# Performance work log

Measured on AMD Instinct MI355X. Metric: run time of the kernel, lower is better.

The kernel has to match this reference:

```python
import jax, jax.numpy as jnp
import numpy as np

N, T, V, F, K, FO = 8, 64, 200, 64, 3, 64


def setup_inputs() -> dict:
    key = jax.random.key(0)
    k1, k2, k3, k4 = jax.random.split(key, 4)
    x = jax.random.normal(k1, (N, T, V, F), dtype=jnp.float32)
    Att = jax.random.uniform(k2, (N, V, V), dtype=jnp.float32)
    S = jax.random.uniform(k3, (N, T, V, V), dtype=jnp.float32)
    Theta = jax.random.normal(k4, (K, F, FO), dtype=jnp.float32) * 0.1
    return {"x": x, "Att": Att, "S": S, "Theta": Theta}


def reference(x, Att, S, Theta):
    # x: (N,T,V,F); Att: (N,V,V); S: (N,T,V,V); Theta: (K,F,FO)
    n, t, v, f = x.shape
    k_order = Theta.shape[0]
    # symmetrize S by elementwise min with its transpose (last two dims)
    S = jnp.minimum(S, jnp.swapaxes(S, -1, -2))
    eye = jnp.eye(v, dtype=x.dtype)
    # D = diag_embed(sum(A, dim=1)) per timestep -> column sums over axis 2
    d = jnp.sum(S, axis=2)                      # (N,T,V)
    L = d[..., :, None] * eye - S               # (N,T,V,V), D - A
    L_t = L - eye                               # tilde-L
    # Chebyshev recursion (elementwise, matching original code exactly)
    polys = [jnp.broadcast_to(eye, (1, 1, v, v)), L_t][:k_order]
    for _ in range(2, k_order):
        polys.append(2.0 * L_t * polys[-1] - polys[-2])
    Att_b = Att[:, None]                        # (N,1,V,V), broadcast over T
    out = jnp.zeros((n, t, v, Theta.shape[-1]), dtype=x.dtype)
    for kk in range(k_order):
        T_k_att = polys[kk] * Att_b             # (N,T,V,V) (broadcast for k=0)
        # rhs = T_k_att^T @ x : sum over vertex u
        rhs = jnp.einsum('...uv,...uf->...vf', T_k_att, x)  # (N,T,V,F)
        out = out + rhs @ Theta[kk]             # (N,T,V,FO)
    return jax.nn.relu(out)
```

## Files before the change

kernel.cpp:

```cpp
#include <hip/hip_runtime.h>

namespace {

typedef __attribute__((ext_vector_type(8)))  short          short8;
typedef __attribute__((ext_vector_type(8)))  unsigned short u16x8;
typedef __attribute__((ext_vector_type(4)))  unsigned short u16x4;
typedef __attribute__((ext_vector_type(4)))  float          f32x4;

constexpr int V  = 200;
constexpr int F  = 64;
constexpr int NT = 512;
constexpr int VP = 208;

constexpr size_t WS_AC  = 0;
constexpr size_t WS_XTF = 95420416;
constexpr size_t WS_THT = 110100480;
constexpr size_t WS_D   = 110125056;
constexpr size_t WS_ADG = 110551040;

__device__ __forceinline__ unsigned short f2bf(float x) {
    union { float f; unsigned u; } c; c.f = x;
    unsigned r = c.u + 0x7FFF + ((c.u >> 16) & 1);
    return (unsigned short)(r >> 16);
}

__global__ __launch_bounds__(256)
void prep_misc(const float* __restrict__ x,
               const float* __restrict__ Theta,
               unsigned short* __restrict__ xTf,
               unsigned short* __restrict__ thT)
{
    __shared__ __align__(16) char smem[30464];
    const int bb = blockIdx.x, tid = threadIdx.x;
    if (bb < NT) {
        unsigned short* xs = (unsigned short*)smem;
        const float* __restrict__ xp = x + (size_t)bb * (V * F);
        for (int idx = tid; idx < 224 * 16; idx += 256) {
            const int u = idx >> 4, fg = idx & 15;
            u16x4 w; w[0] = 0; w[1] = 0; w[2] = 0; w[3] = 0;
            if (u < V) {
                const float4 v4 = *(const float4*)&xp[u * F + 4 * fg];
                w[0] = f2bf(v4.x); w[1] = f2bf(v4.y); w[2] = f2bf(v4.z); w[3] = f2bf(v4.w);
            }
            *(u16x4*)&xs[u * 68 + 4 * fg] = w;
        }
        __syncthreads();
        unsigned short* xo = xTf + (size_t)bb * 14336;
        for (int it = 0; it < 7; ++it) {
            const int wid = tid + 256 * it;
            const int frag = wid >> 6, lane = wid & 63;
            const int kt = frag >> 2, ft = frag & 3;
            const int q = lane >> 4, ln = lane & 15;
            u16x8 w;
            #pragma unroll
            for (int j = 0; j < 8; ++j)
                w[j] = xs[(32 * kt + 8 * q + j) * 68 + 16 * ft + ln];
            *(u16x8*)&xo[frag * 512 + lane * 8] = w;
        }
    } else {
        float* T = (float*)smem;
        for (int k = 0; k < 3; ++k) {
            __syncthreads();
            for (int idx = tid; idx < 4096; idx += 256)
                T[(idx >> 6) * 65 + (idx & 63)] = Theta[k * 4096 + idx];
            __syncthreads();
            for (int idx = tid; idx < 4096; idx += 256) {
                const int fo = idx >> 6, f = idx & 63;
                thT[k * 4096 + fo * 64 + f] = f2bf(T[f * 65 + fo]);
            }
        }
    }
}

__global__ __launch_bounds__(256)
void prep_A(const float* __restrict__ S,
            const float* __restrict__ Att,
            unsigned short* __restrict__ Ac,
            float* __restrict__ d_ws,
            float* __restrict__ adiag)
{
    __shared__ float As[32][33];
    __shared__ float Bs[32][33];
    __shared__ float Ts[32][33];
    __shared__ float Us[32][33];
    __shared__ float Ms[32][33];

    const int b = blockIdx.x, n = b >> 6, tid = threadIdx.x;
    int rem = blockIdx.y, ti = 0;
    while (rem >= 7 - ti) { rem -= 7 - ti; ++ti; }
    const int tj = ti + rem;
    const bool diag = (ti == tj);

    const float* __restrict__ Sp = S   + (size_t)b * (V * V);
    const float* __restrict__ Ap = Att + (size_t)n * (V * V);

    const int r = tid >> 3, cg = tid & 7, c0 = 4 * cg;

    {
        const int gr = 32 * ti + r, gc = 32 * tj + c0;
        float4 a = make_float4(0.f, 0.f, 0.f, 0.f);
        float4 t = make_float4(0.f, 0.f, 0.f, 0.f);
        if (gr < V && gc < V) {
            a = *(const float4*)&Sp[gr * V + gc];
            t = *(const float4*)&Ap[gr * V + gc];
        }
        As[r][c0+0] = a.x; As[r][c0+1] = a.y; As[r][c0+2] = a.z; As[r][c0+3] = a.w;
        Ts[r][c0+0] = t.x; Ts[r][c0+1] = t.y; Ts[r][c0+2] = t.z; Ts[r][c0+3] = t.w;
        if (!diag) {
            const int hr = 32 * tj + r, hc = 32 * ti + c0;
            float4 bb = make_float4(0.f, 0.f, 0.f, 0.f);
            float4 uu = make_float4(0.f, 0.f, 0.f, 0.f);
            if (hr < V && hc < V) {
                bb = *(const float4*)&Sp[hr * V + hc];
                uu = *(const float4*)&Ap[hr * V + hc];
            }
            Bs[r][c0+0] = bb.x; Bs[r][c0+1] = bb.y; Bs[r][c0+2] = bb.z; Bs[r][c0+3] = bb.w;
            Us[r][c0+0] = uu.x; Us[r][c0+1] = uu.y; Us[r][c0+2] = uu.z; Us[r][c0+3] = uu.w;
        }
    }
    __syncthreads();

    {
        float rs = 0.f;
        #pragma unroll
        for (int e = 0; e < 4; ++e) {
            const int c = c0 + e;
            const float tw = diag ? As[c][r] : Bs[c][r];
            const float m = fminf(As[r][c], tw);
            Ms[r][c] = m;
            rs += m;
        }
        rs += __shfl_xor(rs, 1); rs += __shfl_xor(rs, 2); rs += __shfl_xor(rs, 4);
        const int vg = 32 * ti + r;
        if (cg == 0 && vg < V) {
            const float extra = diag ? (-1.0f - As[r][r]) : 0.0f;
            atomicAdd(&d_ws[b * VP + vg], rs + extra);
            if (diag) adiag[n * VP + vg] = Ts[r][r];
        }
    }
    __syncthreads();

    if (!diag) {
        float ts = 0.f;
        #pragma unroll
        for (int e = 0; e < 4; ++e) ts += Ms[c0 + e][r];
        ts += __shfl_xor(ts, 1); ts += __shfl_xor(ts, 2); ts += __shfl_xor(ts, 4);
        if (cg == 0 && 32 * tj + r < V)
            atomicAdd(&d_ws[b * VP + 32 * tj + r], ts);
    }

    const int jh = tid & 1, lane = (tid >> 1) & 63, sub = tid >> 7;
    const int rr = lane & 15, qq = lane >> 4;
    const int vl = sub * 16 + rr;
    const int ub = 8 * qq + 4 * jh;

    if (2 * ti + sub < 13) {
        u16x4 w1, w2;
        #pragma unroll
        for (int e = 0; e < 4; ++e) {
            const int ul = ub + e;
            const float m   = Ms[vl][ul];
            const float att = diag ? Ts[ul][vl] : Us[ul][vl];
            const bool dz = diag && (ul == vl);
            w1[e] = f2bf(dz ? 0.f : -m * att);
            w2[e] = f2bf(dz ? 0.f : 2.0f * m * m * att);
        }
        const size_t base = ((size_t)(b * 13 + 2 * ti + sub) * 7 + tj) * 1024;
        *(u16x4*)&Ac[base +       lane * 8 + jh * 4] = w1;
        *(u16x4*)&Ac[base + 512 + lane * 8 + jh * 4] = w2;
    }
    if (!diag && 2 * tj + sub < 13) {
        u16x4 w1, w2;
        #pragma unroll
        for (int e = 0; e < 4; ++e) {
            const int ul = ub + e;
            const float m   = Ms[ul][vl];
            const float att = Ts[ul][vl];
            w1[e] = f2bf(-m * att);
            w2[e] = f2bf(2.0f * m * m * att);
        }
        const size_t base = ((size_t)(b * 13 + 2 * tj + sub) * 7 + ti) * 1024;
        *(u16x4*)&Ac[base +       lane * 8 + jh * 4] = w1;
        *(u16x4*)&Ac[base + 512 + lane * 8 + jh * 4] = w2;
    }
}

__global__ __launch_bounds__(256, 4)
void cheb_stream(const float* __restrict__ x,
                 const unsigned short* __restrict__ Ac,
                 const float* __restrict__ d_ws,
                 const float* __restrict__ adiag,
                 const unsigned short* __restrict__ thT,
                 const unsigned short* __restrict__ xTf,
                 float* __restrict__ out)
{
    __shared__ __align__(16) char smem[29696];
    unsigned short* xTs = (unsigned short*)smem;
    unsigned short* ys  = (unsigned short*)smem;
    unsigned short* ThS = (unsigned short*)(smem + 16128);
    float* dbuf = (float*)(smem + 28672);
    float* adb  = (float*)(smem + 29120);

    const int tid = threadIdx.x;
    const int ub_ = blockIdx.x;
    const int h   = (ub_ >> 3) & 1;
    const int b   = (ub_ & 7) | ((ub_ >> 4) << 3);
    const int n   = b >> 6;
    const int v0  = h * 112;

    const unsigned short* __restrict__ xfp = xTf + (size_t)b * 14336;
    #pragma unroll
    for (int it = 0; it < 7; ++it) {
        const int o = it * 2048 + tid * 8;
        *(u16x8*)&xTs[o] = *(const u16x8*)&xfp[o];
    }
    if (tid < 112) {
        const int gv = v0 + tid;
        dbuf[tid] = (gv < VP) ? d_ws[b * VP + gv] : 0.f;
        adb[tid]  = (gv < VP) ? adiag[n * VP + gv] : 0.f;
    }

    const int wave = tid >> 6, lane = tid & 63, q = lane >> 4, ln = lane & 15;
    int myBase, myCnt;
    if (h == 0) { myCnt = (wave < 3) ? 2 : 1; myBase = 2 * wave; }
    else        { myCnt = (wave < 2) ? 2 : 1; myBase = (wave < 2) ? 2 * wave : 2 + wave; }

    const float* __restrict__ xp = x + (size_t)b * (V * F);
    float* __restrict__ op = out + (size_t)b * (V * F);

    f32x4 acc1[2][4], acc2[2][4];
    #pragma unroll
    for (int i = 0; i < 2; ++i)
        #pragma unroll
        for (int j = 0; j < 4; ++j) { acc1[i][j] = (f32x4)0.f; acc2[i][j] = (f32x4)0.f; }

    size_t fb0 = ((size_t)(b * 13 + 7 * h + myBase) * 7) * 1024 + lane * 8;
    size_t fb1 = ((size_t)(b * 13 + 7 * h + myBase + 1) * 7) * 1024 + lane * 8;

    short8 a1c[2], a2c[2], a1n[2], a2n[2];
    a1c[0] = *(const short8*)&Ac[fb0];
    a2c[0] = *(const short8*)&Ac[fb0 + 512];
    if (myCnt > 1) {
        a1c[1] = *(const short8*)&Ac[fb1];
        a2c[1] = *(const short8*)&Ac[fb1 + 512];
    }
    __syncthreads();

    #pragma unroll 1
    for (int kt = 0; kt < 7; ++kt) {
        if (kt < 6) {
            const size_t o = (size_t)(kt + 1) * 1024;
            a1n[0] = *(const short8*)&Ac[fb0 + o];
            a2n[0] = *(const short8*)&Ac[fb0 + o + 512];
            if (myCnt > 1) {
                a1n[1] = *(const short8*)&Ac[fb1 + o];
                a2n[1] = *(const short8*)&Ac[fb1 + o + 512];
            }
        }
        short8 bfr[4];
        #pragma unroll
        for (int ft = 0; ft < 4; ++ft)
            bfr[ft] = *(const short8*)&xTs[(kt * 4 + ft) * 512 + lane * 8];
        #pragma unroll
        for (int vi = 0; vi < 2; ++vi) {
            if (vi < myCnt) {
                #pragma unroll
                for (int ft = 0; ft < 4; ++ft) {
                    acc1[vi][ft] = __builtin_amdgcn_mfma_f32_16x16x32_bf16(a1c[vi], bfr[ft], acc1[vi][ft], 0, 0, 0);
                    acc2[vi][ft] = __builtin_amdgcn_mfma_f32_16x16x32_bf16(a2c[vi], bfr[ft], acc2[vi][ft], 0, 0, 0);
                }
            }
        }
        #pragma unroll
        for (int vi = 0; vi < 2; ++vi) { a1c[vi] = a1n[vi]; a2c[vi] = a2n[vi]; }
    }

    f32x4 ot[2][4];
    #pragma unroll
    for (int i = 0; i < 2; ++i)
        #pragma unroll
        for (int j = 0; j < 4; ++j) ot[i][j] = (f32x4)0.f;

    #pragma unroll
    for (int pass = 0; pass < 3; ++pass) {
        const int k = (pass == 0) ? 1 : (pass == 1) ? 2 : 0;
        __syncthreads();

        if (k == 0) {
            for (int idx = tid; idx < 112 * 16; idx += 256) {
                const int vl = idx >> 4, fg = idx & 15;
                const int v = v0 + vl;
                u16x4 w; w[0] = 0; w[1] = 0; w[2] = 0; w[3] = 0;
                if (v < V && vl < 112) {
                    const float av = adb[vl];
                    const float4 xv = *(const float4*)&xp[v * F + 4 * fg];
                    w[0] = f2bf(av * xv.x); w[1] = f2bf(av * xv.y);
                    w[2] = f2bf(av * xv.z); w[3] = f2bf(av * xv.w);
                }
                *(u16x4*)&ys[vl * 72 + 4 * fg] = w;
            }
        } else {
            #pragma unroll
            for (int vi = 0; vi < 2; ++vi) {
                if (vi < myCnt) {
                    const int lt = myBase + vi;
                    #pragma unroll
                    for (int ft = 0; ft < 4; ++ft) {
                        const f32x4 a = (k == 1) ? acc1[vi][ft] : acc2[vi][ft];
                        #pragma unroll
                        for (int reg = 0; reg < 4; ++reg) {
                            const int vl = lt * 16 + 4 * q + reg;
                            const int v = v0 + vl;
                            float val = 0.f;
                            if (v < V) {
                                const float cc = dbuf[vl];
                                const float dc = ((k == 1) ? cc : (2.0f * cc * cc - 1.0f)) * adb[vl];
                                val = a[reg] + dc * xp[v * F + 16 * ft + ln];
                            }
                            ys[vl * 72 + 16 * ft + ln] = f2bf(val);
                        }
                    }
                }
            }
        }
        for (int idx = tid; idx < 512; idx += 256) {
            const int fo = idx >> 3, ch = idx & 7;
            *(u16x8*)&ThS[fo * 72 + 8 * ch] =
                *(const u16x8*)&thT[k * 4096 + fo * 64 + 8 * ch];
        }
        __syncthreads();
        #pragma unroll
        for (int vi = 0; vi < 2; ++vi) {
            if (vi < myCnt) {
                const int vrow = (myBase + vi) * 16 + ln;
                #pragma unroll
                for (int ks = 0; ks < 2; ++ks) {
                    const short8 af = *(const short8*)&ys[vrow * 72 + 32 * ks + 8 * q];
                    #pragma unroll
                    for (int fot = 0; fot < 4; ++fot) {
                        const short8 bf = *(const short8*)&ThS[(16 * fot + ln) * 72 + 32 * ks + 8 * q];
                        ot[vi][fot] = __builtin_amdgcn_mfma_f32_16x16x32_bf16(af, bf, ot[vi][fot], 0, 0, 0);
                    }
                }
            }
        }
    }

    #pragma unroll
    for (int vi = 0; vi < 2; ++vi) {
        if (vi < myCnt) {
            const int lt = myBase + vi;
            #pragma unroll
            for (int fot = 0; fot < 4; ++fot) {
                #pragma unroll
                for (int reg = 0; reg < 4; ++reg) {
                    const int v = v0 + lt * 16 + 4 * q + reg;
                    if (v < V)
                        op[v * F + 16 * fot + ln] = fmaxf(ot[vi][fot][reg], 0.f);
                }
            }
        }
    }
}

}

extern "C" void kernel_launch(void* const* d_in, const int* in_sizes, int n_in,
                              void* d_out, int out_size, void* d_ws, size_t ws_size,
                              hipStream_t stream) {
    const float* x     = (const float*)d_in[0];
    const float* Att   = (const float*)d_in[1];
    const float* S     = (const float*)d_in[2];
    const float* Theta = (const float*)d_in[3];
    float* out         = (float*)d_out;

    char* ws = (char*)d_ws;
    unsigned short* Ac  = (unsigned short*)(ws + WS_AC);
    unsigned short* xTf = (unsigned short*)(ws + WS_XTF);
    unsigned short* thT = (unsigned short*)(ws + WS_THT);
    float* d_sum        = (float*)(ws + WS_D);
    float* adiag        = (float*)(ws + WS_ADG);

    hipMemsetAsync(d_sum, 0, (size_t)NT * VP * sizeof(float), stream);

    hipLaunchKernelGGL(prep_misc,   dim3(NT + 1), dim3(256), 0, stream, x, Theta, xTf, thT);
    hipLaunchKernelGGL(prep_A,      dim3(NT, 28), dim3(256), 0, stream, S, Att, Ac, d_sum, adiag);
    hipLaunchKernelGGL(cheb_stream, dim3(2 * NT), dim3(256), 0, stream,
                       x, Ac, d_sum, adiag, thT, xTf, out);
}
```

Baseline: 233.5 us.

## Store symmetrized S and Att in fp16, rebuild Chebyshev operands in-register

```diff
diff --git a/kernel.cpp b/kernel.cpp
--- a/kernel.cpp
+++ b/kernel.cpp
@@ -6,17 +6,20 @@
 typedef __attribute__((ext_vector_type(8)))  unsigned short u16x8;
 typedef __attribute__((ext_vector_type(4)))  unsigned short u16x4;
 typedef __attribute__((ext_vector_type(4)))  float          f32x4;
+typedef __attribute__((ext_vector_type(8)))  _Float16       half8;
+typedef __attribute__((ext_vector_type(4)))  _Float16       half4;
 
 constexpr int V  = 200;
 constexpr int F  = 64;
 constexpr int NT = 512;
 constexpr int VP = 208;
 
-constexpr size_t WS_AC  = 0;
-constexpr size_t WS_XTF = 95420416;
-constexpr size_t WS_THT = 110100480;
-constexpr size_t WS_D   = 110125056;
-constexpr size_t WS_ADG = 110551040;
+constexpr size_t WS_MC   = 0;
+constexpr size_t WS_XTF  = 47710208;
+constexpr size_t WS_ATTF = 62390272;
+constexpr size_t WS_THT  = 63135744;
+constexpr size_t WS_D    = 63160320;
+constexpr size_t WS_ADG  = 63586304;
 
 __device__ __forceinline__ unsigned short f2bf(float x) {
     union { float f; unsigned u; } c; c.f = x;
@@ -25,42 +28,50 @@
 }
 
 __global__ __launch_bounds__(256)
-void prep_misc(const float* __restrict__ x,
-               const float* __restrict__ Theta,
-               unsigned short* __restrict__ xTf,
-               unsigned short* __restrict__ thT)
+void prep_all(const float* __restrict__ S,
+              const float* __restrict__ Att,
+              const float* __restrict__ x,
+              const float* __restrict__ Theta,
+              _Float16* __restrict__ Mc,
+              _Float16* __restrict__ attF,
+              _Float16* __restrict__ xTf,
+              unsigned short* __restrict__ thT,
+              float* __restrict__ d_ws,
+              float* __restrict__ adiag)
 {
     __shared__ __align__(16) char smem[30464];
-    const int bb = blockIdx.x, tid = threadIdx.x;
-    if (bb < NT) {
-        unsigned short* xs = (unsigned short*)smem;
-        const float* __restrict__ xp = x + (size_t)bb * (V * F);
+    const int b = blockIdx.x, n = b >> 6, tid = threadIdx.x;
+
+    if (blockIdx.y == 28) {
+        _Float16* xs = (_Float16*)smem;
+        const float* __restrict__ xp = x + (size_t)b * (V * F);
         for (int idx = tid; idx < 224 * 16; idx += 256) {
             const int u = idx >> 4, fg = idx & 15;
-            u16x4 w; w[0] = 0; w[1] = 0; w[2] = 0; w[3] = 0;
+            half4 w = (half4)(_Float16)0.f;
             if (u < V) {
                 const float4 v4 = *(const float4*)&xp[u * F + 4 * fg];
-                w[0] = f2bf(v4.x); w[1] = f2bf(v4.y); w[2] = f2bf(v4.z); w[3] = f2bf(v4.w);
-            }
-            *(u16x4*)&xs[u * 68 + 4 * fg] = w;
+                w[0] = (_Float16)v4.x; w[1] = (_Float16)v4.y;
+                w[2] = (_Float16)v4.z; w[3] = (_Float16)v4.w;
+            }
+            *(half4*)&xs[u * 68 + 4 * fg] = w;
         }
         __syncthreads();
-        unsigned short* xo = xTf + (size_t)bb * 14336;
+        _Float16* xo = xTf + (size_t)b * 14336;
         for (int it = 0; it < 7; ++it) {
             const int wid = tid + 256 * it;
             const int frag = wid >> 6, lane = wid & 63;
             const int kt = frag >> 2, ft = frag & 3;
             const int q = lane >> 4, ln = lane & 15;
-            u16x8 w;
+            half8 w;
             #pragma unroll
             for (int j = 0; j < 8; ++j)
                 w[j] = xs[(32 * kt + 8 * q + j) * 68 + 16 * ft + ln];
-            *(u16x8*)&xo[frag * 512 + lane * 8] = w;
-        }
-    } else {
-        float* T = (float*)smem;
-        for (int k = 0; k < 3; ++k) {
+            *(half8*)&xo[frag * 512 + lane * 8] = w;
+        }
+        if (b < 3) {
+            const int k = b;
             __syncthreads();
+            float* T = (float*)smem;
             for (int idx = tid; idx < 4096; idx += 256)
                 T[(idx >> 6) * 65 + (idx & 63)] = Theta[k * 4096 + idx];
             __syncthreads();
@@ -69,23 +80,15 @@
                 thT[k * 4096 + fo * 64 + f] = f2bf(T[f * 65 + fo]);
             }
         }
-    }
-}
-
-__global__ __launch_bounds__(256)
-void prep_A(const float* __restrict__ S,
-            const float* __restrict__ Att,
-            unsigned short* __restrict__ Ac,
-            float* __restrict__ d_ws,
-            float* __restrict__ adiag)
-{
-    __shared__ float As[32][33];
-    __shared__ float Bs[32][33];
-    __shared__ float Ts[32][33];
-    __shared__ float Us[32][33];
-    __shared__ float Ms[32][33];
-
-    const int b = blockIdx.x, n = b >> 6, tid = threadIdx.x;
+        return;
+    }
+
+    float (*As)[33] = (float(*)[33])smem;
+    float (*Bs)[33] = (float(*)[33])(smem + 4224);
+    float (*Ts)[33] = (float(*)[33])(smem + 8448);
+    float (*Us)[33] = (float(*)[33])(smem + 12672);
+    float (*Ms)[33] = (float(*)[33])(smem + 16896);
+
     int rem = blockIdx.y, ti = 0;
     while (rem >= 7 - ti) { rem -= 7 - ti; ++ti; }
     const int tj = ti + rem;
@@ -153,49 +156,53 @@
     const int rr = lane & 15, qq = lane >> 4;
     const int vl = sub * 16 + rr;
     const int ub = 8 * qq + 4 * jh;
+    const bool wAtt = ((b & 63) == 0);
 
     if (2 * ti + sub < 13) {
-        u16x4 w1, w2;
+        half4 wm, wa;
         #pragma unroll
         for (int e = 0; e < 4; ++e) {
             const int ul = ub + e;
-            const float m   = Ms[vl][ul];
+            wm[e] = (_Float16)Ms[vl][ul];
             const float att = diag ? Ts[ul][vl] : Us[ul][vl];
-            const bool dz = diag && (ul == vl);
-            w1[e] = f2bf(dz ? 0.f : -m * att);
-            w2[e] = f2bf(dz ? 0.f : 2.0f * m * m * att);
-        }
-        const size_t base = ((size_t)(b * 13 + 2 * ti + sub) * 7 + tj) * 1024;
-        *(u16x4*)&Ac[base +       lane * 8 + jh * 4] = w1;
-        *(u16x4*)&Ac[base + 512 + lane * 8 + jh * 4] = w2;
+            wa[e] = (diag && ul == vl) ? (_Float16)0.f : (_Float16)att;
+        }
+        const size_t base = ((size_t)(b * 13 + 2 * ti + sub) * 7 + tj) * 512 + lane * 8 + jh * 4;
+        *(half4*)&Mc[base] = wm;
+        if (wAtt) {
+            const size_t ab = ((size_t)(n * 13 + 2 * ti + sub) * 7 + tj) * 512 + lane * 8 + jh * 4;
+            *(half4*)&attF[ab] = wa;
+        }
     }
     if (!diag && 2 * tj + sub < 13) {
-        u16x4 w1, w2;
+        half4 wm, wa;
         #pragma unroll
         for (int e = 0; e < 4; ++e) {
             const int ul = ub + e;
-            const float m   = Ms[ul][vl];
-            const float att = Ts[ul][vl];
-            w1[e] = f2bf(-m * att);
-            w2[e] = f2bf(2.0f * m * m * att);
-        }
-        const size_t base = ((size_t)(b * 13 + 2 * tj + sub) * 7 + ti) * 1024;
-        *(u16x4*)&Ac[base +       lane * 8 + jh * 4] = w1;
-        *(u16x4*)&Ac[base + 512 + lane * 8 + jh * 4] = w2;
+            wm[e] = (_Float16)Ms[ul][vl];
+            wa[e] = (_Float16)Ts[ul][vl];
+        }
+        const size_t base = ((size_t)(b * 13 + 2 * tj + sub) * 7 + ti) * 512 + lane * 8 + jh * 4;
+        *(half4*)&Mc[base] = wm;
+        if (wAtt) {
+            const size_t ab = ((size_t)(n * 13 + 2 * tj + sub) * 7 + ti) * 512 + lane * 8 + jh * 4;
+            *(half4*)&attF[ab] = wa;
+        }
     }
 }
 
 __global__ __launch_bounds__(256, 4)
 void cheb_stream(const float* __restrict__ x,
-                 const unsigned short* __restrict__ Ac,
+                 const _Float16* __restrict__ Mc,
+                 const _Float16* __restrict__ attF,
                  const float* __restrict__ d_ws,
                  const float* __restrict__ adiag,
                  const unsigned short* __restrict__ thT,
-                 const unsigned short* __restrict__ xTf,
+                 const _Float16* __restrict__ xTf,
                  float* __restrict__ out)
 {
     __shared__ __align__(16) char smem[29696];
-    unsigned short* xTs = (unsigned short*)smem;
+    _Float16*       xTs = (_Float16*)smem;
     unsigned short* ys  = (unsigned short*)smem;
     unsigned short* ThS = (unsigned short*)(smem + 16128);
     float* dbuf = (float*)(smem + 28672);
@@ -208,11 +215,11 @@
     const int n   = b >> 6;
     const int v0  = h * 112;
 
-    const unsigned short* __restrict__ xfp = xTf + (size_t)b * 14336;
+    const _Float16* __restrict__ xfp = xTf + (size_t)b * 14336;
     #pragma unroll
     for (int it = 0; it < 7; ++it) {
         const int o = it * 2048 + tid * 8;
-        *(u16x8*)&xTs[o] = *(const u16x8*)&xfp[o];
+        *(half8*)&xTs[o] = *(const half8*)&xfp[o];
     }
     if (tid < 112) {
         const int gv = v0 + tid;
@@ -234,45 +241,50 @@
         #pragma unroll
         for (int j = 0; j < 4; ++j) { acc1[i][j] = (f32x4)0.f; acc2[i][j] = (f32x4)0.f; }
 
-    size_t fb0 = ((size_t)(b * 13 + 7 * h + myBase) * 7) * 1024 + lane * 8;
-    size_t fb1 = ((size_t)(b * 13 + 7 * h + myBase + 1) * 7) * 1024 + lane * 8;
-
-    short8 a1c[2], a2c[2], a1n[2], a2n[2];
-    a1c[0] = *(const short8*)&Ac[fb0];
-    a2c[0] = *(const short8*)&Ac[fb0 + 512];
+    const size_t fb0 = ((size_t)(b * 13 + 7 * h + myBase) * 7) * 512 + lane * 8;
+    const size_t fb1 = fb0 + 7 * 512;
+    const size_t af0 = ((size_t)(n * 13 + 7 * h + myBase) * 7) * 512 + lane * 8;
+    const size_t af1 = af0 + 7 * 512;
+
+    half8 mc[2] = {}, ac[2] = {}, mn[2] = {}, an[2] = {};
+    mc[0] = *(const half8*)&Mc[fb0];
+    ac[0] = *(const half8*)&attF[af0];
     if (myCnt > 1) {
-        a1c[1] = *(const short8*)&Ac[fb1];
-        a2c[1] = *(const short8*)&Ac[fb1 + 512];
+        mc[1] = *(const half8*)&Mc[fb1];
+        ac[1] = *(const half8*)&attF[af1];
     }
     __syncthreads();
 
     #pragma unroll 1
     for (int kt = 0; kt < 7; ++kt) {
         if (kt < 6) {
-            const size_t o = (size_t)(kt + 1) * 1024;
-            a1n[0] = *(const short8*)&Ac[fb0 + o];
-            a2n[0] = *(const short8*)&Ac[fb0 + o + 512];
+            const size_t o = (size_t)(kt + 1) * 512;
+            mn[0] = *(const half8*)&Mc[fb0 + o];
+            an[0] = *(const half8*)&attF[af0 + o];
             if (myCnt > 1) {
-                a1n[1] = *(const short8*)&Ac[fb1 + o];
-                a2n[1] = *(const short8*)&Ac[fb1 + o + 512];
-            }
-        }
-        short8 bfr[4];
+                mn[1] = *(const half8*)&Mc[fb1 + o];
+                an[1] = *(const half8*)&attF[af1 + o];
+            }
+        }
+        half8 bfr[4];
         #pragma unroll
         for (int ft = 0; ft < 4; ++ft)
-            bfr[ft] = *(const short8*)&xTs[(kt * 4 + ft) * 512 + lane * 8];
+            bfr[ft] = *(const half8*)&xTs[(kt * 4 + ft) * 512 + lane * 8];
         #pragma unroll
         for (int vi = 0; vi < 2; ++vi) {
             if (vi < myCnt) {
+                const half8 t  = mc[vi] * ac[vi];
+                const half8 a1 = -t;
+                const half8 a2 = (mc[vi] + mc[vi]) * t;
                 #pragma unroll
                 for (int ft = 0; ft < 4; ++ft) {
-                    acc1[vi][ft] = __builtin_amdgcn_mfma_f32_16x16x32_bf16(a1c[vi], bfr[ft], acc1[vi][ft], 0, 0, 0);
-                    acc2[vi][ft] = __builtin_amdgcn_mfma_f32_16x16x32_bf16(a2c[vi], bfr[ft], acc2[vi][ft], 0, 0, 0);
+                    acc1[vi][ft] = __builtin_amdgcn_mfma_f32_16x16x32_f16(a1, bfr[ft], acc1[vi][ft], 0, 0, 0);
+                    acc2[vi][ft] = __builtin_amdgcn_mfma_f32_16x16x32_f16(a2, bfr[ft], acc2[vi][ft], 0, 0, 0);
                 }
             }
         }
         #pragma unroll
-        for (int vi = 0; vi < 2; ++vi) { a1c[vi] = a1n[vi]; a2c[vi] = a2n[vi]; }
+        for (int vi = 0; vi < 2; ++vi) { mc[vi] = mn[vi]; ac[vi] = an[vi]; }
     }
 
     f32x4 ot[2][4];
@@ -291,7 +303,7 @@
                 const int vl = idx >> 4, fg = idx & 15;
                 const int v = v0 + vl;
                 u16x4 w; w[0] = 0; w[1] = 0; w[2] = 0; w[3] = 0;
-                if (v < V && vl < 112) {
+                if (v < V) {
                     const float av = adb[vl];
                     const float4 xv = *(const float4*)&xp[v * F + 4 * fg];
                     w[0] = f2bf(av * xv.x); w[1] = f2bf(av * xv.y);
@@ -375,16 +387,17 @@
     float* out         = (float*)d_out;
 
     char* ws = (char*)d_ws;
-    unsigned short* Ac  = (unsigned short*)(ws + WS_AC);
-    unsigned short* xTf = (unsigned short*)(ws + WS_XTF);
+    _Float16* Mc        = (_Float16*)(ws + WS_MC);
+    _Float16* xTf       = (_Float16*)(ws + WS_XTF);
+    _Float16* attF      = (_Float16*)(ws + WS_ATTF);
     unsigned short* thT = (unsigned short*)(ws + WS_THT);
     float* d_sum        = (float*)(ws + WS_D);
     float* adiag        = (float*)(ws + WS_ADG);
 
     hipMemsetAsync(d_sum, 0, (size_t)NT * VP * sizeof(float), stream);
 
-    hipLaunchKernelGGL(prep_misc,   dim3(NT + 1), dim3(256), 0, stream, x, Theta, xTf, thT);
-    hipLaunchKernelGGL(prep_A,      dim3(NT, 28), dim3(256), 0, stream, S, Att, Ac, d_sum, adiag);
+    hipLaunchKernelGGL(prep_all, dim3(NT, 29), dim3(256), 0, stream,
+                       S, Att, x, Theta, Mc, attF, xTf, thT, d_sum, adiag);
     hipLaunchKernelGGL(cheb_stream, dim3(2 * NT), dim3(256), 0, stream,
-                       x, Ac, d_sum, adiag, thT, xTf, out);
+                       x, Mc, attF, d_sum, adiag, thT, xTf, out);
 }
```

Measured after the change: 212.4 us. 9.0% less time.
